# Kernel tuning notes

Hardware: AMD Instinct MI355X
Metric: run time of the kernel (lower is better)

The kernel has to match this reference:

```python
import jax, jax.numpy as jnp
import numpy as np

B, N, C, P, HEADS = 4, 1024, 128, 4, 16
D = P * P * C          # 2048 token feature dim
DH = D // HEADS        # 128 per-head dim
MASK_NUM = 25
SCALE = 64 ** (-0.5)   # hardcoded in the original module


def setup_inputs() -> dict:
    key = jax.random.key(0)
    ks = jax.random.split(key, 12)
    s = 0.05
    return {
        "x": jax.random.normal(ks[0], (B, N, D), jnp.float32),
        "Wq": jax.random.normal(ks[1], (C, C), jnp.float32) * s,
        "bq": jax.random.normal(ks[2], (C,), jnp.float32) * s,
        "Wk": jax.random.normal(ks[3], (C, C), jnp.float32) * s,
        "bk": jax.random.normal(ks[4], (C,), jnp.float32) * s,
        "Wv": jax.random.normal(ks[5], (C, C), jnp.float32) * s,
        "bv": jax.random.normal(ks[6], (C,), jnp.float32) * s,
        "Wl": jax.random.normal(ks[7], (1, C), jnp.float32) * s,
        "bl": jax.random.normal(ks[8], (1,), jnp.float32) * s,
        "Wo": jax.random.normal(ks[9], (D, D), jnp.float32) * (1.0 / np.sqrt(D)),
        "bo": jax.random.normal(ks[10], (D,), jnp.float32) * s,
        "stage": 0,
    }


def reference(x, Wq, bq, Wk, bk, Wv, bv, Wl, bl, Wo, bo, stage):
    b, n, d = x.shape
    # 1x1 conv over the channel axis is a per-position linear map; the
    # token<->image rearranges are layout-only, so apply it directly on
    # (b, n, p*p, C).
    xr = x.reshape(b, n, P * P, C)
    q = jnp.einsum('bnpc,oc->bnpo', xr, Wq) + bq   # conv_q (1x1)
    k = jnp.einsum('bnpc,oc->bnpo', xr, Wk) + bk   # conv_k (1x1)
    v = jnp.einsum('bnpc,oc->bnpo', xr, Wv) + bv   # conv_v (1x1)

    # Token-importance mask: avg over the p*p positions (AdaptiveAvgPool2d
    # (1, C)), linear C->1, softmax over tokens.
    m = q.mean(axis=2)                              # (b, n, C)
    logits = (m @ Wl.T + bl)[..., 0]                # (b, n)
    mask = jax.nn.softmax(logits, axis=-1)
    # threshold = mask_num-th smallest value per row; values strictly above
    # it are snapped to 1, the rest keep their (tiny) softmax value.
    thr = -jax.lax.top_k(-mask, MASK_NUM)[0][..., -1:]   # (b, 1)... per-row
    mask = jnp.where(mask > thr, jnp.float32(1.0), mask)  # (b, n)

    kf = k.reshape(b, n, d) * mask[:, :, None]
    vf = v.reshape(b, n, d) * mask[:, :, None]

    qh = q.reshape(b, n, HEADS, DH).transpose(0, 2, 1, 3)   # (b, h, n, dh)
    kh = kf.reshape(b, n, HEADS, DH).transpose(0, 2, 1, 3)
    vh = vf.reshape(b, n, HEADS, DH).transpose(0, 2, 1, 3)

    dots = jnp.einsum('bhid,bhjd->bhij', qh, kh) * SCALE
    attn = jax.nn.softmax(dots, axis=-1)
    out = jnp.einsum('bhij,bhjd->bhid', attn, vh)
    out = out.transpose(0, 2, 1, 3).reshape(b, n, d)
    return out @ Wo.T + bo                          # to_out (dropout p=0)
```

## Files before the change

kernel.cpp:

```cpp
#include <hip/hip_runtime.h>
#include <stdint.h>

typedef __attribute__((ext_vector_type(8))) short s8v;
typedef __attribute__((ext_vector_type(4))) short s4v;
typedef __attribute__((ext_vector_type(4))) float f4v;

#define MFMA(a,b,c) __builtin_amdgcn_mfma_f32_16x16x32_bf16((a),(b),(c),0,0,0)

__device__ __forceinline__ short f2bf(float f){
  union { float f; unsigned u; } a; a.f = f;
  unsigned r = (a.u + 0x7fffu + ((a.u >> 16) & 1u)) >> 16;
  return (short)r;
}
__device__ __forceinline__ unsigned pkt(float lo, float hi){
  return __builtin_amdgcn_perm(__float_as_uint(hi), __float_as_uint(lo), 0x07060302);
}

__device__ __forceinline__ void gld16(const void* g, void* l){
  __builtin_amdgcn_global_load_lds((const __attribute__((address_space(1))) void*)g,
                                   (__attribute__((address_space(3))) void*)l, 16, 0, 0);
}

__global__ void k_prep(const float* __restrict__ Wq, const float* __restrict__ Wk,
                       const float* __restrict__ Wv, const float* __restrict__ Wo,
                       const float* __restrict__ bq, const float* __restrict__ Wl,
                       const float* __restrict__ bl,
                       short* __restrict__ wq16, short* __restrict__ wk16,
                       short* __restrict__ wv16, short* __restrict__ wo16,
                       float* __restrict__ wcomb){
  int i = blockIdx.x*256 + threadIdx.x;
  wo16[i] = f2bf(Wo[i]);
  if (i < 16384){ wq16[i] = f2bf(Wq[i]); wk16[i] = f2bf(Wk[i]); wv16[i] = f2bf(Wv[i]); }
  if (blockIdx.x == 0 && threadIdx.x < 128){
    int c = threadIdx.x;
    float s = 0.f;
    for (int o = 0; o < 128; ++o) s += Wl[o] * Wq[o*128 + c];
    wcomb[c] = s;
    if (c == 0){
      float t = 0.f; for (int o = 0; o < 128; ++o) t += Wl[o] * bq[o];
      wcomb[128] = t + bl[0];
    }
  }
}

__global__ __launch_bounds__(256) void k_conv_x(const float* __restrict__ x, const float* __restrict__ wcomb,
                                                short* __restrict__ x16, float* __restrict__ logits){
  __shared__ float wc[128];
  __shared__ float part[4];
  int t = blockIdx.x, tid = threadIdx.x;
  if (tid < 128) wc[tid] = wcomb[tid];
  __syncthreads();
  const float* xp = x + (size_t)t*2048;
  short* op = x16 + (size_t)t*2048;
  float s = 0.f;
  #pragma unroll
  for (int j = 0; j < 2; ++j){
    int idx = j*1024 + tid*4;
    float4 v = *(const float4*)(xp + idx);
    s4v o; o.x = f2bf(v.x); o.y = f2bf(v.y); o.z = f2bf(v.z); o.w = f2bf(v.w);
    *(s4v*)(op + idx) = o;
    s += v.x*wc[idx&127] + v.y*wc[(idx+1)&127] + v.z*wc[(idx+2)&127] + v.w*wc[(idx+3)&127];
  }
  for (int off = 32; off; off >>= 1) s += __shfl_down(s, off);
  if ((tid&63) == 0) part[tid>>6] = s;
  __syncthreads();
  if (tid == 0) logits[t] = (part[0]+part[1]+part[2]+part[3])*(1.f/16.f) + wcomb[128];
}

__global__ __launch_bounds__(64) void k_mask(const float* __restrict__ logits, float* __restrict__ maskout){
  int b = blockIdx.x, lane = threadIdx.x;
  float v[16];
  #pragma unroll
  for (int i = 0; i < 16; ++i) v[i] = logits[b*1024 + i*64 + lane];
  float mx = v[0];
  #pragma unroll
  for (int i = 1; i < 16; ++i) mx = fmaxf(mx, v[i]);
  #pragma unroll
  for (int off = 32; off; off >>= 1) mx = fmaxf(mx, __shfl_xor(mx, off));
  float s = 0.f;
  #pragma unroll
  for (int i = 0; i < 16; ++i){ v[i] = __expf(v[i] - mx); s += v[i]; }
  #pragma unroll
  for (int off = 32; off; off >>= 1) s += __shfl_xor(s, off);
  float p[16];
  #pragma unroll
  for (int i = 0; i < 16; ++i){ p[i] = v[i] / s; v[i] = p[i]; }
  float thr = 0.f;
  for (int k = 0; k < 25; ++k){
    float lm = v[0]; int li = 0;
    #pragma unroll
    for (int i = 1; i < 16; ++i){ if (v[i] < lm){ lm = v[i]; li = i; } }
    float gm = lm;
    #pragma unroll
    for (int off = 32; off; off >>= 1) gm = fminf(gm, __shfl_xor(gm, off));
    if (k == 24) thr = gm;
    unsigned long long ball = __ballot(lm == gm);
    int owner = __ffsll((unsigned long long)ball) - 1;
    bool rm = (lane == owner);
    #pragma unroll
    for (int i = 0; i < 16; ++i){ if (rm && i == li) v[i] = 2.0f; }
  }
  #pragma unroll
  for (int i = 0; i < 16; ++i)
    maskout[b*1024 + i*64 + lane] = p[i] > thr ? 1.0f : p[i];
}

__global__ __launch_bounds__(256) void k_qkv3(const short* __restrict__ x16,
                                              const short* __restrict__ wq16, const short* __restrict__ wk16,
                                              const short* __restrict__ wv16,
                                              const float* __restrict__ bq, const float* __restrict__ bk,
                                              const float* __restrict__ bv, const float* __restrict__ maskp,
                                              short* __restrict__ q16, short* __restrict__ k16,
                                              short* __restrict__ vt16){
  __shared__ short At[64*136];
  __shared__ short Wt[128*136];
  int tid = threadIdx.x, lane = tid&63, w = tid>>6;
  int n0 = blockIdx.x*64, p = blockIdx.y, b = blockIdx.z;
  #pragma unroll
  for (int i = 0; i < 4; ++i){
    int ch = tid + 256*i; int r = ch>>4, c8 = (ch&15)*8;
    *(s8v*)&At[r*136 + c8] = *(const s8v*)(x16 + (size_t)(b*1024 + n0 + r)*2048 + p*128 + c8);
  }
  int ln = lane&15, q = lane>>4;
  float mvr[4];
  #pragma unroll
  for (int r = 0; r < 4; ++r) mvr[r] = maskp[b*1024 + n0 + w*16 + q*4 + r];
  const short* ws[3] = {wq16, wk16, wv16};
  const float* bs[3] = {bq, bk, bv};
  for (int ps = 0; ps < 3; ++ps){
    if (ps) __syncthreads();
    #pragma unroll
    for (int i = 0; i < 8; ++i){
      int ch = tid + 256*i; int r = ch>>4, c8 = (ch&15)*8;
      *(s8v*)&Wt[r*136 + c8] = *(const s8v*)(ws[ps] + r*128 + c8);
    }
    __syncthreads();
    f4v acc[8];
    #pragma unroll
    for (int cb = 0; cb < 8; ++cb) acc[cb] = f4v{0.f,0.f,0.f,0.f};
    #pragma unroll
    for (int ks = 0; ks < 4; ++ks){
      s8v a = *(const s8v*)&At[(w*16+ln)*136 + ks*32 + q*8];
      #pragma unroll
      for (int cb = 0; cb < 8; ++cb){
        s8v bb = *(const s8v*)&Wt[(cb*16+ln)*136 + ks*32 + q*8];
        acc[cb] = MFMA(a, bb, acc[cb]);
      }
    }
    const float* bp = bs[ps];
    if (ps < 2){
      float sc = (ps == 0) ? 0.180336881f : 1.0f;
      short* op = (ps == 0) ? q16 : k16;
      #pragma unroll
      for (int cb = 0; cb < 8; ++cb){
        int col = cb*16 + ln;
        float bv2 = bp[col];
        #pragma unroll
        for (int r = 0; r < 4; ++r){
          int n = n0 + w*16 + q*4 + r;
          float mm = (ps == 1) ? mvr[r] : 1.0f;
          op[(size_t)(b*1024 + n)*2048 + p*128 + col] = f2bf((acc[cb][r] + bv2)*sc*mm);
        }
      }
    } else {
      __syncthreads();
      #pragma unroll
      for (int cb = 0; cb < 8; ++cb){
        int col = cb*16 + ln;
        float bv2 = bp[col];
        #pragma unroll
        for (int r = 0; r < 4; ++r)
          At[(w*16 + q*4 + r)*136 + col] = f2bf((acc[cb][r] + bv2)*mvr[r]);
      }
      __syncthreads();
      #pragma unroll
      for (int i = 0; i < 4; ++i){
        int ch = tid + 256*i; int c = ch>>3, n8 = (ch&7)*8;
        s8v o;
        #pragma unroll
        for (int j = 0; j < 8; ++j) o[j] = At[(n8+j)*136 + c];
        *(s8v*)(vt16 + (size_t)((b*16+p)*128 + c)*1024 + n0 + n8) = o;
      }
    }
  }
}

__global__ __launch_bounds__(256, 2) void k_attn(const short* __restrict__ q16, const short* __restrict__ k16,
                                                 const short* __restrict__ vt16, short* __restrict__ a16){
  __shared__ short Ks[64*128];
  __shared__ short Vs[128*64];
  __shared__ short Ps[128*72];
  int h = blockIdx.x, it = blockIdx.y, b = blockIdx.z;
  int i0 = it*128;
  int tid = threadIdx.x, lane = tid&63, w = tid>>6;
  int ln = lane&15, q = lane>>4;
  s8v aq[2][4];
  const short* qbase = q16 + (size_t)(b*1024 + i0 + w*32)*2048 + h*128;
  #pragma unroll
  for (int g = 0; g < 2; ++g)
    #pragma unroll
    for (int ks = 0; ks < 4; ++ks)
      aq[g][ks] = *(const s8v*)(qbase + (size_t)(g*16+ln)*2048 + ks*32 + q*8);
  s8v ones;
  #pragma unroll
  for (int j = 0; j < 8; ++j) ones[j] = (short)0x3F80;
  f4v o[2][8], o9[2];
  #pragma unroll
  for (int g = 0; g < 2; ++g){
    #pragma unroll
    for (int cb = 0; cb < 8; ++cb) o[g][cb] = f4v{0.f,0.f,0.f,0.f};
    o9[g] = f4v{0.f,0.f,0.f,0.f};
  }
  float mo[2] = {-3.0e38f, -3.0e38f};
  const short* kbase = k16 + (size_t)(b*1024)*2048 + h*128;
  const short* vbase = vt16 + (size_t)((b*16+h)*128)*1024;
  for (int jt = 0; jt < 16; ++jt){
    int j0 = jt*64;
    __syncthreads();
    #pragma unroll
    for (int t = 0; t < 4; ++t){
      int r = w*16 + t*4 + (lane>>4);
      int c = lane&15;
      gld16(kbase + (size_t)(j0 + r)*2048 + ((c ^ (r&7))*8), &Ks[(w*16 + t*4)*128]);
    }
    #pragma unroll
    for (int t = 0; t < 4; ++t){
      int r = w*32 + t*8 + (lane>>3);
      int c = lane&7;
      gld16(vbase + (size_t)r*1024 + j0 + ((c ^ (r&7))*8), &Vs[(w*32 + t*8)*64]);
    }
    __syncthreads();
    f4v st[2][4];
    #pragma unroll
    for (int g = 0; g < 2; ++g)
      #pragma unroll
      for (int mb = 0; mb < 4; ++mb) st[g][mb] = f4v{0.f,0.f,0.f,0.f};
    #pragma unroll
    for (int ks = 0; ks < 4; ++ks)
      #pragma unroll
      for (int mb = 0; mb < 4; ++mb){
        s8v ka = *(const s8v*)&Ks[(mb*16+ln)*128 + (((ks*4 + q) ^ (ln&7))*8)];
        st[0][mb] = MFMA(ka, aq[0][ks], st[0][mb]);
        st[1][mb] = MFMA(ka, aq[1][ks], st[1][mb]);
      }
    float alv[2];
    #pragma unroll
    for (int g = 0; g < 2; ++g){
      float mx = st[g][0][0];
      #pragma unroll
      for (int mb = 0; mb < 4; ++mb)
        #pragma unroll
        for (int r = 0; r < 4; ++r) mx = fmaxf(mx, st[g][mb][r]);
      mx = fmaxf(mx, __shfl_xor(mx, 16));
      mx = fmaxf(mx, __shfl_xor(mx, 32));
      float mnew = fmaxf(mo[g], mx);
      alv[g] = exp2f(mo[g] - mnew);
      mo[g] = mnew;
      int prow = (w*32 + g*16 + ln)*72;
      #pragma unroll
      for (int mb = 0; mb < 4; ++mb){
        uint2 u;
        u.x = pkt(exp2f(st[g][mb][0] - mnew), exp2f(st[g][mb][1] - mnew));
        u.y = pkt(exp2f(st[g][mb][2] - mnew), exp2f(st[g][mb][3] - mnew));
        *(uint2*)&Ps[prow + mb*16 + q*4] = u;
      }
    }
    float alr[2][4];
    #pragma unroll
    for (int g = 0; g < 2; ++g)
      #pragma unroll
      for (int r = 0; r < 4; ++r) alr[g][r] = __shfl(alv[g], q*4 + r);
    #pragma unroll
    for (int g = 0; g < 2; ++g){
      #pragma unroll
      for (int cb = 0; cb < 8; ++cb)
        #pragma unroll
        for (int r = 0; r < 4; ++r) o[g][cb][r] *= alr[g][r];
      #pragma unroll
      for (int r = 0; r < 4; ++r) o9[g][r] *= alr[g][r];
    }
    __syncthreads();
    #pragma unroll
    for (int ks = 0; ks < 2; ++ks){
      s8v pa[2];
      #pragma unroll
      for (int g = 0; g < 2; ++g) pa[g] = *(const s8v*)&Ps[(w*32 + g*16 + ln)*72 + ks*32 + q*8];
      #pragma unroll
      for (int cb = 0; cb < 8; ++cb){
        s8v bb = *(const s8v*)&Vs[(cb*16+ln)*64 + (((ks*4 + q) ^ (ln&7))*8)];
        o[0][cb] = MFMA(pa[0], bb, o[0][cb]);
        o[1][cb] = MFMA(pa[1], bb, o[1][cb]);
      }
      o9[0] = MFMA(pa[0], ones, o9[0]);
      o9[1] = MFMA(pa[1], ones, o9[1]);
    }
  }
  #pragma unroll
  for (int g = 0; g < 2; ++g)
    #pragma unroll
    for (int cb = 0; cb < 8; ++cb){
      int col = cb*16 + ln;
      #pragma unroll
      for (int r = 0; r < 4; ++r){
        int row = i0 + w*32 + g*16 + q*4 + r;
        a16[(size_t)(b*1024 + row)*2048 + h*128 + col] = f2bf(o[g][cb][r] / o9[g][r]);
      }
    }
}

__global__ __launch_bounds__(256) void k_out(const short* __restrict__ a16, const short* __restrict__ wo16,
                                             const float* __restrict__ bo, float* __restrict__ out){
  __shared__ short As[128*64];
  __shared__ short Bs[128*64];
  int tid = threadIdx.x, lane = tid&63, w = tid>>6;
  int m0 = blockIdx.x*128, n0 = blockIdx.y*128;
  int wrow = (w>>1)*64, wcol = (w&1)*64;
  int ln = lane&15, q = lane>>4;
  f4v acc[4][4];
  #pragma unroll
  for (int i = 0; i < 4; ++i)
    #pragma unroll
    for (int j = 0; j < 4; ++j) acc[i][j] = f4v{0.f,0.f,0.f,0.f};
  for (int it = 0; it < 32; ++it){
    int k0 = it*64;
    __syncthreads();
    #pragma unroll
    for (int t = 0; t < 4; ++t){
      int r = w*32 + t*8 + (lane>>3);
      int c = lane&7;
      int gc8 = (c ^ (r&7))*8;
      gld16(a16  + (size_t)(m0+r)*2048 + k0 + gc8, &As[(w*32 + t*8)*64]);
      gld16(wo16 + (size_t)(n0+r)*2048 + k0 + gc8, &Bs[(w*32 + t*8)*64]);
    }
    __syncthreads();
    #pragma unroll
    for (int ks = 0; ks < 2; ++ks){
      s8v a[4], bb[4];
      int swz = ((ks*4 + q) ^ (ln&7))*8;
      #pragma unroll
      for (int i = 0; i < 4; ++i){
        a[i]  = *(const s8v*)&As[(wrow + i*16 + ln)*64 + swz];
        bb[i] = *(const s8v*)&Bs[(wcol + i*16 + ln)*64 + swz];
      }
      #pragma unroll
      for (int i = 0; i < 4; ++i)
        #pragma unroll
        for (int j = 0; j < 4; ++j) acc[i][j] = MFMA(a[i], bb[j], acc[i][j]);
    }
  }
  #pragma unroll
  for (int j = 0; j < 4; ++j){
    int col = n0 + wcol + j*16 + ln;
    float bv = bo[col];
    #pragma unroll
    for (int i = 0; i < 4; ++i)
      #pragma unroll
      for (int r = 0; r < 4; ++r){
        int row = m0 + wrow + i*16 + q*4 + r;
        out[(size_t)row*2048 + col] = acc[i][j][r] + bv;
      }
  }
}

extern "C" void kernel_launch(void* const* d_in, const int* in_sizes, int n_in,
                              void* d_out, int out_size, void* d_ws, size_t ws_size,
                              hipStream_t stream){
  const float* x  = (const float*)d_in[0];
  const float* Wq = (const float*)d_in[1];
  const float* bq = (const float*)d_in[2];
  const float* Wk = (const float*)d_in[3];
  const float* bk = (const float*)d_in[4];
  const float* Wv = (const float*)d_in[5];
  const float* bv = (const float*)d_in[6];
  const float* Wl = (const float*)d_in[7];
  const float* bl = (const float*)d_in[8];
  const float* Wo = (const float*)d_in[9];
  const float* bo = (const float*)d_in[10];
  float* out = (float*)d_out;

  char* p = (char*)d_ws;
  size_t off = 0;
  auto take = [&](size_t bytes)->char*{ char* r = p + off; off = (off + bytes + 255) & ~(size_t)255; return r; };
  short* x16   = (short*)take(16777216);
  short* q16   = (short*)take(16777216);
  short* k16   = (short*)take(16777216);
  short* vt16  = (short*)take(16777216);
  short* wo16  = (short*)take(8388608);
  short* wq16  = (short*)take(32768);
  short* wk16  = (short*)take(32768);
  short* wv16  = (short*)take(32768);
  float* wcomb = (float*)take(4*129);
  float* logits= (float*)take(4*4096);
  float* maskp = (float*)take(4*4096);
  short* a16 = x16;

  k_prep  <<<16384, 256, 0, stream>>>(Wq, Wk, Wv, Wo, bq, Wl, bl, wq16, wk16, wv16, wo16, wcomb);
  k_conv_x<<<4096, 256, 0, stream>>>(x, wcomb, x16, logits);
  k_mask  <<<4, 64, 0, stream>>>(logits, maskp);
  k_qkv3  <<<dim3(16, 16, 4), 256, 0, stream>>>(x16, wq16, wk16, wv16, bq, bk, bv, maskp, q16, k16, vt16);
  k_attn  <<<dim3(16, 8, 4), 256, 0, stream>>>(q16, k16, vt16, a16);
  k_out   <<<dim3(32, 16), 256, 0, stream>>>(a16, wo16, bo, out);
}
```

Baseline: 257.3 us.

## Prefetch next K/V and GEMM tiles into registers instead of direct LDS loads

The attention and output-projection kernels no longer use global_load_lds. Each thread now loads the next tile's K/V (or A/Wo) fragments into registers while the current tile is being computed, then writes them to LDS after the barrier. This is meant to overlap global memory latency with MFMA work. The attention loop also drops one barrier before the P·V phase, since each wave only reads its own P rows. The cost is extra VGPRs for the staging registers and an explicit LDS store pass, which may reduce occupancy.

```diff
diff --git a/kernel.cpp b/kernel.cpp
--- a/kernel.cpp
+++ b/kernel.cpp
@@ -14,11 +14,6 @@
 }
 __device__ __forceinline__ unsigned pkt(float lo, float hi){
   return __builtin_amdgcn_perm(__float_as_uint(hi), __float_as_uint(lo), 0x07060302);
-}
-
-__device__ __forceinline__ void gld16(const void* g, void* l){
-  __builtin_amdgcn_global_load_lds((const __attribute__((address_space(1))) void*)g,
-                                   (__attribute__((address_space(3))) void*)l, 16, 0, 0);
 }
 
 __global__ void k_prep(const float* __restrict__ Wq, const float* __restrict__ Wk,
@@ -214,22 +209,43 @@
   float mo[2] = {-3.0e38f, -3.0e38f};
   const short* kbase = k16 + (size_t)(b*1024)*2048 + h*128;
   const short* vbase = vt16 + (size_t)((b*16+h)*128)*1024;
+  s8v kr[4], vr[4];
+  #pragma unroll
+  for (int t = 0; t < 4; ++t){
+    int r = w*16 + t*4 + (lane>>4), c = lane&15;
+    kr[t] = *(const s8v*)(kbase + (size_t)r*2048 + ((c ^ (r&7))*8));
+  }
+  #pragma unroll
+  for (int t = 0; t < 4; ++t){
+    int r = w*32 + t*8 + (lane>>3), c = lane&7;
+    vr[t] = *(const s8v*)(vbase + (size_t)r*1024 + ((c ^ (r&7))*8));
+  }
   for (int jt = 0; jt < 16; ++jt){
-    int j0 = jt*64;
     __syncthreads();
     #pragma unroll
     for (int t = 0; t < 4; ++t){
-      int r = w*16 + t*4 + (lane>>4);
-      int c = lane&15;
-      gld16(kbase + (size_t)(j0 + r)*2048 + ((c ^ (r&7))*8), &Ks[(w*16 + t*4)*128]);
+      int r = w*16 + t*4 + (lane>>4), c = lane&15;
+      *(s8v*)&Ks[r*128 + c*8] = kr[t];
     }
     #pragma unroll
     for (int t = 0; t < 4; ++t){
-      int r = w*32 + t*8 + (lane>>3);
-      int c = lane&7;
-      gld16(vbase + (size_t)r*1024 + j0 + ((c ^ (r&7))*8), &Vs[(w*32 + t*8)*64]);
+      int r = w*32 + t*8 + (lane>>3), c = lane&7;
+      *(s8v*)&Vs[r*64 + c*8] = vr[t];
     }
     __syncthreads();
+    if (jt < 15){
+      int j0n = (jt+1)*64;
+      #pragma unroll
+      for (int t = 0; t < 4; ++t){
+        int r = w*16 + t*4 + (lane>>4), c = lane&15;
+        kr[t] = *(const s8v*)(kbase + (size_t)(j0n + r)*2048 + ((c ^ (r&7))*8));
+      }
+      #pragma unroll
+      for (int t = 0; t < 4; ++t){
+        int r = w*32 + t*8 + (lane>>3), c = lane&7;
+        vr[t] = *(const s8v*)(vbase + (size_t)r*1024 + j0n + ((c ^ (r&7))*8));
+      }
+    }
     f4v st[2][4];
     #pragma unroll
     for (int g = 0; g < 2; ++g)
@@ -279,7 +295,6 @@
       #pragma unroll
       for (int r = 0; r < 4; ++r) o9[g][r] *= alr[g][r];
     }
-    __syncthreads();
     #pragma unroll
     for (int ks = 0; ks < 2; ++ks){
       s8v pa[2];
@@ -321,18 +336,33 @@
   for (int i = 0; i < 4; ++i)
     #pragma unroll
     for (int j = 0; j < 4; ++j) acc[i][j] = f4v{0.f,0.f,0.f,0.f};
+  s8v ar[4], br[4];
+  #pragma unroll
+  for (int t = 0; t < 4; ++t){
+    int r = w*32 + t*8 + (lane>>3), c = lane&7;
+    int gc8 = (c ^ (r&7))*8;
+    ar[t] = *(const s8v*)(a16  + (size_t)(m0+r)*2048 + gc8);
+    br[t] = *(const s8v*)(wo16 + (size_t)(n0+r)*2048 + gc8);
+  }
   for (int it = 0; it < 32; ++it){
-    int k0 = it*64;
     __syncthreads();
     #pragma unroll
     for (int t = 0; t < 4; ++t){
-      int r = w*32 + t*8 + (lane>>3);
-      int c = lane&7;
-      int gc8 = (c ^ (r&7))*8;
-      gld16(a16  + (size_t)(m0+r)*2048 + k0 + gc8, &As[(w*32 + t*8)*64]);
-      gld16(wo16 + (size_t)(n0+r)*2048 + k0 + gc8, &Bs[(w*32 + t*8)*64]);
+      int r = w*32 + t*8 + (lane>>3), c = lane&7;
+      *(s8v*)&As[r*64 + c*8] = ar[t];
+      *(s8v*)&Bs[r*64 + c*8] = br[t];
     }
     __syncthreads();
+    if (it < 31){
+      int k0 = (it+1)*64;
+      #pragma unroll
+      for (int t = 0; t < 4; ++t){
+        int r = w*32 + t*8 + (lane>>3), c = lane&7;
+        int gc8 = (c ^ (r&7))*8;
+        ar[t] = *(const s8v*)(a16  + (size_t)(m0+r)*2048 + k0 + gc8);
+        br[t] = *(const s8v*)(wo16 + (size_t)(n0+r)*2048 + k0 + gc8);
+      }
+    }
     #pragma unroll
     for (int ks = 0; ks < 2; ++ks){
       s8v a[4], bb[4];
```

Result: no change. 258.6 us (+0.5%).
